# Kernel optimization log

Measured on AMD Instinct MI355X. Metric: run time of the kernel, lower is better.

The kernel has to match this reference:

```python
import jax, jax.numpy as jnp
import numpy as np
import math

D_IN, D_MODEL, N_HEADS, N_LAYERS, D_FF = 128, 256, 4, 4, 1024
NUM_BANDS = D_MODEL // 6  # 42 -> 252 encoding dims, zero-padded to 256
LN_EPS = 1e-5


def setup_inputs() -> dict:
    key = jax.random.key(0)
    ks = jax.random.split(key, 32)
    N, B = 65536, 128
    s = 0.02
    L, D, F = N_LAYERS, D_MODEL, D_FF
    inp = {
        "dom_embeddings": jax.random.normal(ks[0], (N, D_IN), jnp.float32),
        "dom_to_event_idx": jnp.sort(jax.random.randint(ks[1], (N,), 0, B)),
        "batch_size": B,
        "geometry": jax.random.normal(ks[2], (N, 3), jnp.float32),
        "in_proj_w": jax.random.normal(ks[3], (D, D_IN), jnp.float32) * s,
        "in_proj_b": jnp.zeros((D,), jnp.float32),
        "geo_proj_w": jax.random.normal(ks[4], (D, D), jnp.float32) * s,
        "geo_proj_b": jnp.zeros((D,), jnp.float32),
        "cls_token": jax.random.normal(ks[5], (1, 1, D), jnp.float32),
        "qkv_w": jax.random.normal(ks[6], (L, 3 * D, D), jnp.float32) * s,
        "qkv_b": jnp.zeros((L, 3 * D), jnp.float32),
        "out_w": jax.random.normal(ks[7], (L, D, D), jnp.float32) * s,
        "out_b": jnp.zeros((L, D), jnp.float32),
        "ln1_w": jnp.ones((L, D), jnp.float32),
        "ln1_b": jnp.zeros((L, D), jnp.float32),
        "ln2_w": jnp.ones((L, D), jnp.float32),
        "ln2_b": jnp.zeros((L, D), jnp.float32),
        "ff_w1": jax.random.normal(ks[8], (L, F, D), jnp.float32) * s,
        "ff_b1": jnp.zeros((L, F), jnp.float32),
        "ff_w2": jax.random.normal(ks[9], (L, D, F), jnp.float32) * s,
        "ff_b2": jnp.zeros((L, D), jnp.float32),
        "head_w1": jax.random.normal(ks[10], (D, D), jnp.float32) * s,
        "head_b1": jnp.zeros((D,), jnp.float32),
        "head_w2": jax.random.normal(ks[11], (2, D), jnp.float32) * s,
        "head_b2": jnp.zeros((2,), jnp.float32),
    }
    return inp


def _layer_norm(x, w, b):
    m = x.mean(-1, keepdims=True)
    v = ((x - m) ** 2).mean(-1, keepdims=True)
    return (x - m) / jnp.sqrt(v + LN_EPS) * w + b


def _pos_enc(geometry):
    # geometry: (N,3). Order: per coord -> per freq -> [sin, cos]; pad to D_MODEL.
    freqs = jnp.logspace(0.0, 1.0, NUM_BANDS, dtype=jnp.float32)  # 1..max_freq=10
    ang = 2.0 * math.pi * geometry[:, :, None] * freqs[None, None, :]  # (N,3,F)
    sc = jnp.stack([jnp.sin(ang), jnp.cos(ang)], axis=-1)  # (N,3,F,2)
    enc = sc.reshape(geometry.shape[0], 3 * NUM_BANDS * 2)  # (N,252)
    pad = D_MODEL - enc.shape[1]
    return jnp.pad(enc, ((0, 0), (0, pad)))


def _self_attn(x, pad_mask, Wqkv, bqkv, Wo, bo):
    B, S, D = x.shape
    H, hd = N_HEADS, D // N_HEADS
    qkv = x @ Wqkv.T + bqkv  # (B,S,3D)
    q, k, v = jnp.split(qkv, 3, axis=-1)
    q = q.reshape(B, S, H, hd).transpose(0, 2, 1, 3)
    k = k.reshape(B, S, H, hd).transpose(0, 2, 1, 3)
    v = v.reshape(B, S, H, hd).transpose(0, 2, 1, 3)
    scores = jnp.einsum('bhqd,bhkd->bhqk', q, k) / math.sqrt(hd)
    scores = jnp.where(pad_mask[:, None, None, :], -jnp.inf, scores)
    a = jax.nn.softmax(scores, axis=-1)
    o = jnp.einsum('bhqk,bhkd->bhqd', a, v).transpose(0, 2, 1, 3).reshape(B, S, D)
    return o @ Wo.T + bo


def reference(dom_embeddings, dom_to_event_idx, batch_size, geometry,
              in_proj_w, in_proj_b, geo_proj_w, geo_proj_b, cls_token,
              qkv_w, qkv_b, out_w, out_b, ln1_w, ln1_b, ln2_w, ln2_b,
              ff_w1, ff_b1, ff_w2, ff_b2, head_w1, head_b1, head_w2, head_b2):
    N = dom_embeddings.shape[0]
    B = int(batch_size)
    x = dom_embeddings @ in_proj_w.T + in_proj_b  # (N,D)
    geo = _pos_enc(geometry) @ geo_proj_w.T + geo_proj_b
    x = x + geo

    # Vectorized scatter-pack (replaces per-DOM Python loop).
    counts = jnp.bincount(dom_to_event_idx, length=B)
    starts = jnp.concatenate([jnp.zeros((1,), counts.dtype), jnp.cumsum(counts)[:-1]])
    pos = jnp.arange(N) - starts[dom_to_event_idx] + 1  # slot 0 reserved for CLS
    max_doms = int(counts.max())
    S = max_doms + 1

    batch_tensor = jnp.zeros((B, S, D_MODEL), x.dtype)
    batch_tensor = batch_tensor.at[:, 0, :].set(cls_token[0, 0])
    batch_tensor = batch_tensor.at[dom_to_event_idx, pos].set(x)
    # True = padded. NOTE: CLS slot stays True, faithful to original code.
    pad_mask = jnp.ones((B, S), bool).at[dom_to_event_idx, pos].set(False)

    h = batch_tensor
    for l in range(N_LAYERS):  # pre-LN encoder layers
        h = h + _self_attn(_layer_norm(h, ln1_w[l], ln1_b[l]), pad_mask,
                           qkv_w[l], qkv_b[l], out_w[l], out_b[l])
        ff_in = _layer_norm(h, ln2_w[l], ln2_b[l])
        h = h + jax.nn.relu(ff_in @ ff_w1[l].T + ff_b1[l]) @ ff_w2[l].T + ff_b2[l]

    cls = h[:, 0, :]
    hid = jax.nn.relu(cls @ head_w1.T + head_b1)
    return hid @ head_w2.T + head_b2  # (B,2)
```

## Files before the change

kernel.cpp:

```cpp
#include <hip/hip_runtime.h>
#include <hip/hip_bf16.h>
#include <math.h>


#define D_INPUT  128
#define DM       256
#define NHEADS   4
#define HDIM     64
#define NLAYERS  4
#define DFF      1024
#define BEV      128
#define LNEPS    1e-5f
#define KT       10
#define SCL      0.18033688011112042f

typedef unsigned short u16;
typedef __attribute__((ext_vector_type(8))) short bf16x8;
typedef __attribute__((ext_vector_type(4))) float f32x4;

__device__ inline u16 f2bf(float x) {
    unsigned int xi = __float_as_uint(x);
    unsigned int r  = xi + 0x7FFFu + ((xi >> 16) & 1u);
    return (u16)(r >> 16);
}
__device__ inline unsigned int cvtpk(float lo, float hi) {
    unsigned int r;
    asm("v_cvt_pk_bf16_f32 %0, %1, %2" : "=v"(r) : "v"(lo), "v"(hi));
    return r;
}

__device__ inline size_t apack(int row, int col, int nkt) {
    return ((size_t)(row >> 4) * nkt + (col >> 6)) * 1024
         + ((col >> 5) & 1) * 512
         + ((((col >> 3) & 3) * 16 + (row & 15)) * 8) + (col & 7);
}
__device__ inline size_t wpack_off(int col, int k, int nkt) {
    const int c16 = col >> 4, llo = col & 15;
    const int kt = k >> 6, kr = k & 63;
    const int kk = kr >> 5, lhi = (kr >> 3) & 3, e = kr & 7;
    return ((size_t)(c16 * nkt + kt)) * 1024 + kk * 512 + (lhi * 16 + llo) * 8 + e;
}


__global__ void starts_kernel(const int* __restrict__ idx, int* __restrict__ counts,
                              int* __restrict__ starts, int N) {
    __shared__ int bnd[BEV + 1];
    const int b = threadIdx.x;
    if (b <= BEV) {
        int lo = 0, hi = N;
        while (lo < hi) { int mid = (lo + hi) >> 1; if (idx[mid] < b) lo = mid + 1; else hi = mid; }
        bnd[b] = lo;
    }
    __syncthreads();
    if (b < BEV) { starts[b] = bnd[b]; counts[b] = bnd[b + 1] - bnd[b]; }
}

__global__ void r2bs_kernel(const int* __restrict__ idx, const int* __restrict__ starts,
                            int* __restrict__ r2bs, int N, int TP) {
    int i = blockIdx.x * blockDim.x + threadIdx.x;
    if (i < N) {
        int b = idx[i];
        r2bs[i] = (b << 16) | (i - starts[b] + 1);
    } else if (i < N + BEV) {
        r2bs[i] = (i - N) << 16;
    } else if (i < TP) {
        r2bs[i] = BEV << 16;
    }
}

__global__ void beacon_kernel(float* out, int n, float v) {
    int i = blockIdx.x * blockDim.x + threadIdx.x;
    if (i < n) out[i] = v;
}

__global__ void cvt4p_kernel(const float* __restrict__ s0, const float* __restrict__ s1,
                             const float* __restrict__ s2, const float* __restrict__ s3,
                             u16* __restrict__ d0, u16* __restrict__ d1,
                             u16* __restrict__ d2, u16* __restrict__ d3) {
    const int n0 = NLAYERS * 768 * 256, n1 = NLAYERS * 256 * 256;
    const int n2 = NLAYERS * 1024 * 256, n3 = NLAYERS * 256 * 1024;
    int i = blockIdx.x * blockDim.x + threadIdx.x;
    if (i < n0) {
        const int NoK = 768 * 256;
        int l = i / NoK, rem = i - l * NoK, col = rem >> 8, k = rem & 255;
        d0[(size_t)l * NoK + wpack_off(col, k, 4)] = f2bf(s0[i]);
        return;
    }
    i -= n0;
    if (i < n1) {
        const int NoK = 256 * 256;
        int l = i / NoK, rem = i - l * NoK, col = rem >> 8, k = rem & 255;
        d1[(size_t)l * NoK + wpack_off(col, k, 4)] = f2bf(s1[i]);
        return;
    }
    i -= n1;
    if (i < n2) {
        const int NoK = 1024 * 256;
        int l = i / NoK, rem = i - l * NoK, col = rem >> 8, k = rem & 255;
        d2[(size_t)l * NoK + wpack_off(col, k, 4)] = f2bf(s2[i]);
        return;
    }
    i -= n2;
    if (i < n3) {
        const int NoK = 256 * 1024;
        int l = i / NoK, rem = i - l * NoK, col = rem >> 10, k = rem & 1023;
        d3[(size_t)l * NoK + wpack_off(col, k, 16)] = f2bf(s3[i]);
    }
}

__global__ void prep_w_kernel(const float* __restrict__ win, const float* __restrict__ wgeo,
                              const float* __restrict__ bin, const float* __restrict__ bgeo,
                              u16* __restrict__ We, float* __restrict__ be) {
    int i = blockIdx.x * blockDim.x + threadIdx.x;
    if (i < 256 * 384) {
        int o = i / 384, k = i % 384;
        float v = 0.f;
        if (k < 128)      v = win[o * 128 + k];
        else if (k < 380) v = wgeo[o * 256 + (k - 128)];
        We[wpack_off(o, k, 6)] = f2bf(v);
    }
    if (i < 256) be[i] = bin[i] + bgeo[i];
}

__global__ void prep_a_kernel(const float* __restrict__ emb, const float* __restrict__ geo,
                              u16* __restrict__ Ap, int N) {
    size_t t = (size_t)blockIdx.x * blockDim.x + threadIdx.x;
    if (t >= (size_t)N * 96) return;
    const int c4 = (int)(t % 96) * 4;
    const size_t r = t / 96;
    float v[4];
    #pragma unroll
    for (int u = 0; u < 4; ++u) {
        const int k = c4 + u;
        float x = 0.f;
        if (k < 128) {
            x = emb[r * 128 + k];
        } else if (k < 380) {
            int rem  = k - 128;
            int axis = rem / 84;
            int r2   = rem % 84;
            int band = r2 >> 1;
            int sc   = r2 & 1;
            float freq = expf((float)band * (2.3025850929940457f / 41.0f));
            float ang  = (6.283185307179586f * geo[r * 3 + axis]) * freq;
            x = sc ? cosf(ang) : sinf(ang);
        }
        v[u] = x;
    }
    uint2 pp;
    pp.x = cvtpk(v[0], v[1]);
    pp.y = cvtpk(v[2], v[3]);
    *(uint2*)&Ap[apack((int)r, c4, 6)] = pp;
}

__global__ void cls_kernel(const float* __restrict__ cls, float* __restrict__ h, int N) {
    h[(size_t)(N + blockIdx.x) * DM + threadIdx.x] = cls[threadIdx.x];
}


__global__ __launch_bounds__(256) void ln_kernel(const float* __restrict__ x,
                                                 const float* __restrict__ w,
                                                 const float* __restrict__ b,
                                                 u16* __restrict__ yp, int T) {
    int row  = blockIdx.x * 4 + (threadIdx.x >> 6);
    int lane = threadIdx.x & 63;
    if (row >= T) return;
    float4 v = ((const float4*)(x + (size_t)row * DM))[lane];
    float s = v.x + v.y + v.z + v.w;
    #pragma unroll
    for (int off = 32; off > 0; off >>= 1) s += __shfl_xor(s, off);
    float mean = s * (1.0f / 256.0f);
    float dx = v.x - mean, dy = v.y - mean, dz = v.z - mean, dw = v.w - mean;
    float ss = dx * dx + dy * dy + dz * dz + dw * dw;
    #pragma unroll
    for (int off = 32; off > 0; off >>= 1) ss += __shfl_xor(ss, off);
    float inv = rsqrtf(ss * (1.0f / 256.0f) + LNEPS);
    float4 wv = ((const float4*)w)[lane];
    float4 bv = ((const float4*)b)[lane];
    const int col0 = lane * 4;
    uint2 yy;
    yy.x = cvtpk(dx * inv * wv.x + bv.x, dy * inv * wv.y + bv.y);
    yy.y = cvtpk(dz * inv * wv.z + bv.z, dw * inv * wv.w + bv.w);
    *(uint2*)&yp[apack(row, col0, 4)] = yy;
}


template <int MODE>
__global__ __launch_bounds__(256) void pgemm_kernel(const u16* __restrict__ Xp,
                                                    const u16* __restrict__ Wp,
                                                    const float* __restrict__ bias,
                                                    float* __restrict__ C,
                                                    u16* __restrict__ Qb,
                                                    u16* __restrict__ KVt,
                                                    const int* __restrict__ r2bs,
                                                    int nkt) {
    const int m0 = blockIdx.y * 64, n0 = blockIdx.x * 256;
    const int tid = threadIdx.x, wv = tid >> 6, lane = tid & 63;
    const int lhi = lane >> 4, llo = lane & 15;
    const int rt0 = m0 >> 4;

    f32x4 acc[4][4];
    #pragma unroll
    for (int i = 0; i < 4; ++i)
        #pragma unroll
        for (int j = 0; j < 4; ++j) acc[i][j] = (f32x4){0.f, 0.f, 0.f, 0.f};

    for (int kt = 0; kt < nkt; ++kt) {
        #pragma unroll
        for (int kk = 0; kk < 2; ++kk) {
            bf16x8 xf[4], wf[4];
            #pragma unroll
            for (int i = 0; i < 4; ++i)
                xf[i] = *(const bf16x8*)(Xp + ((size_t)(rt0 + i) * nkt + kt) * 1024
                                         + kk * 512 + lane * 8);
            #pragma unroll
            for (int j = 0; j < 4; ++j) {
                const int c16 = (n0 >> 4) + wv * 4 + j;
                wf[j] = *(const bf16x8*)(Wp + ((size_t)c16 * nkt + kt) * 1024
                                         + kk * 512 + lane * 8);
            }
            #pragma unroll
            for (int i = 0; i < 4; ++i)
                #pragma unroll
                for (int j = 0; j < 4; ++j)
                    acc[i][j] = __builtin_amdgcn_mfma_f32_16x16x32_bf16(wf[j], xf[i], acc[i][j], 0, 0, 0);
        }
    }

    #pragma unroll
    for (int i = 0; i < 4; ++i) {
        const int row = m0 + i * 16 + llo;
        int eb = 0, pos = 0, ktile = KT;
        if (MODE == 1 && n0 >= 256) {
            const int bs = r2bs[row];
            eb = bs >> 16; pos = bs & 0xffff; ktile = pos >> 6;
        }
        #pragma unroll
        for (int j = 0; j < 4; ++j) {
            const int col0 = n0 + wv * 64 + j * 16 + lhi * 4;
            const float4 bb = *(const float4*)&bias[col0];
            const float v0 = acc[i][j][0] + bb.x, v1 = acc[i][j][1] + bb.y;
            const float v2 = acc[i][j][2] + bb.z, v3 = acc[i][j][3] + bb.w;
            if (MODE == 0) {
                float4 c = {v0, v1, v2, v3};
                *(float4*)&C[(size_t)row * 256 + col0] = c;
            } else if (MODE == 2) {
                uint2 yy;
                yy.x = cvtpk(fmaxf(v0, 0.f), fmaxf(v1, 0.f));
                yy.y = cvtpk(fmaxf(v2, 0.f), fmaxf(v3, 0.f));
                *(uint2*)&Qb[apack(row, col0, 16)] = yy;
            } else if (n0 == 0) {
                uint2 q;
                q.x = cvtpk(v0 * SCL, v1 * SCL);
                q.y = cvtpk(v2 * SCL, v3 * SCL);
                *(uint2*)&Qb[(size_t)row * 256 + col0] = q;
            } else if (n0 == 256) {
                if (ktile < KT) {
                    const int dg = col0 - 256, hh = dg >> 6, d0 = dg & 63;
                    const int unit = ((pos & 63) >> 4) * 2 + (d0 >> 5);
                    const int lt = ((d0 >> 3) & 3) * 16 + (pos & 15);
                    uint2 pp = {cvtpk(v0, v1), cvtpk(v2, v3)};
                    *(uint2*)&KVt[(((size_t)(eb * 4 + hh) * 2 + 0) * KT + ktile) * 4096
                                  + unit * 512 + lt * 8 + (d0 & 7)] = pp;
                }
            } else {
                if (ktile < KT) {
                    const int dg = col0 - 512, hh = dg >> 6, d0 = dg & 63;
                    const size_t vb = (((size_t)(eb * 4 + hh) * 2 + 1) * KT + ktile) * 4096
                                    + ((d0 >> 4) * 2 + ((pos & 63) >> 5)) * 512
                                    + ((((pos & 63) >> 3) & 3) * 16) * 8 + (pos & 7);
                    KVt[vb + (size_t)((d0 & 15) + 0) * 8] = f2bf(v0);
                    KVt[vb + (size_t)((d0 & 15) + 1) * 8] = f2bf(v1);
                    KVt[vb + (size_t)((d0 & 15) + 2) * 8] = f2bf(v2);
                    KVt[vb + (size_t)((d0 & 15) + 3) * 8] = f2bf(v3);
                }
            }
        }
    }
}


__global__ __launch_bounds__(256) void mgemmln_kernel(const u16* __restrict__ Xp,
                                                      const u16* __restrict__ Wp,
                                                      const float* __restrict__ bias,
                                                      float* __restrict__ H,
                                                      const float* __restrict__ lnw,
                                                      const float* __restrict__ lnb,
                                                      u16* __restrict__ Yp,
                                                      int nkt) {
    __shared__ float part[2][4][64];
    const int m0 = blockIdx.x * 64;
    const int tid = threadIdx.x, wv = tid >> 6, lane = tid & 63;
    const int lhi = lane >> 4, llo = lane & 15;
    const int rt0 = m0 >> 4;

    f32x4 acc[4][4];
    #pragma unroll
    for (int i = 0; i < 4; ++i)
        #pragma unroll
        for (int j = 0; j < 4; ++j) acc[i][j] = (f32x4){0.f, 0.f, 0.f, 0.f};

    for (int kt = 0; kt < nkt; ++kt) {
        #pragma unroll
        for (int kk = 0; kk < 2; ++kk) {
            bf16x8 xf[4], wf[4];
            #pragma unroll
            for (int i = 0; i < 4; ++i)
                xf[i] = *(const bf16x8*)(Xp + ((size_t)(rt0 + i) * nkt + kt) * 1024
                                         + kk * 512 + lane * 8);
            #pragma unroll
            for (int j = 0; j < 4; ++j) {
                const int c16 = wv * 4 + j;
                wf[j] = *(const bf16x8*)(Wp + ((size_t)c16 * nkt + kt) * 1024
                                         + kk * 512 + lane * 8);
            }
            #pragma unroll
            for (int i = 0; i < 4; ++i)
                #pragma unroll
                for (int j = 0; j < 4; ++j)
                    acc[i][j] = __builtin_amdgcn_mfma_f32_16x16x32_bf16(wf[j], xf[i], acc[i][j], 0, 0, 0);
        }
    }

    float rsum[4], rsq[4];
    #pragma unroll
    for (int i = 0; i < 4; ++i) { rsum[i] = 0.f; rsq[i] = 0.f; }
    #pragma unroll
    for (int i = 0; i < 4; ++i) {
        const int row = m0 + i * 16 + llo;
        #pragma unroll
        for (int j = 0; j < 4; ++j) {
            const int col0 = wv * 64 + j * 16 + lhi * 4;
            const float4 bb = *(const float4*)&bias[col0];
            const float4 hv = *(const float4*)&H[(size_t)row * DM + col0];
            float v0 = acc[i][j][0] + bb.x + hv.x;
            float v1 = acc[i][j][1] + bb.y + hv.y;
            float v2 = acc[i][j][2] + bb.z + hv.z;
            float v3 = acc[i][j][3] + bb.w + hv.w;
            acc[i][j][0] = v0; acc[i][j][1] = v1; acc[i][j][2] = v2; acc[i][j][3] = v3;
            rsum[i] += (v0 + v1) + (v2 + v3);
            rsq[i]  += (v0 * v0 + v1 * v1) + (v2 * v2 + v3 * v3);
        }
    }
    #pragma unroll
    for (int i = 0; i < 4; ++i) {
        rsum[i] += __shfl_xor(rsum[i], 16);  rsum[i] += __shfl_xor(rsum[i], 32);
        rsq[i]  += __shfl_xor(rsq[i], 16);   rsq[i]  += __shfl_xor(rsq[i], 32);
    }
    __syncthreads();
    if (lhi == 0) {
        #pragma unroll
        for (int i = 0; i < 4; ++i) {
            const int rl = i * 16 + llo;
            part[0][wv][rl] = rsum[i];
            part[1][wv][rl] = rsq[i];
        }
    }
    __syncthreads();

    #pragma unroll
    for (int i = 0; i < 4; ++i) {
        const int rl = i * 16 + llo;
        const int row = m0 + rl;
        const float s = (part[0][0][rl] + part[0][1][rl]) + (part[0][2][rl] + part[0][3][rl]);
        const float q = (part[1][0][rl] + part[1][1][rl]) + (part[1][2][rl] + part[1][3][rl]);
        const float mean = s * (1.0f / 256.0f);
        const float var  = fmaxf(q * (1.0f / 256.0f) - mean * mean, 0.f);
        const float rstd = rsqrtf(var + LNEPS);
        #pragma unroll
        for (int j = 0; j < 4; ++j) {
            const int col0 = wv * 64 + j * 16 + lhi * 4;
            const float4 wl = *(const float4*)&lnw[col0];
            const float4 bl = *(const float4*)&lnb[col0];
            float4 hv;
            hv.x = acc[i][j][0]; hv.y = acc[i][j][1];
            hv.z = acc[i][j][2]; hv.w = acc[i][j][3];
            *(float4*)&H[(size_t)row * DM + col0] = hv;
            uint2 yy;
            yy.x = cvtpk((hv.x - mean) * rstd * wl.x + bl.x,
                         (hv.y - mean) * rstd * wl.y + bl.y);
            yy.y = cvtpk((hv.z - mean) * rstd * wl.z + bl.z,
                         (hv.w - mean) * rstd * wl.w + bl.w);
            *(uint2*)&Yp[apack(row, col0, 4)] = yy;
        }
    }
}


__global__ __launch_bounds__(256) void mattn_kernel(const u16* __restrict__ Qb,
                                                    const u16* __restrict__ KVt,
                                                    const int* __restrict__ counts,
                                                    const int* __restrict__ starts,
                                                    u16* __restrict__ outp, int N) {
    const int id  = blockIdx.x;
    const int rem = id >> 3;
    const int qt  = rem % KT;
    const int bh  = (rem / KT) * 8 + (id & 7);
    const int b = bh >> 2, hh = bh & 3;
    const int Sb = counts[b] + 1;
    const int qbase = qt * 64;
    if (qbase >= Sb) return;
    const int start = starts[b];
    __shared__ u16 Pl[4][16 * 72];
    const int tid = threadIdx.x;
    const int w = tid >> 6, lane = tid & 63;
    const int llo = lane & 15, lhi = lane >> 4;

    const int qi = qbase + w * 16 + llo;
    const size_t qrow = (qi < Sb && qi > 0) ? (size_t)(start + qi - 1) : (size_t)(N + b);
    bf16x8 bq[2];
    bq[0] = *(const bf16x8*)(Qb + qrow * 256 + hh * 64 + lhi * 8);
    bq[1] = *(const bf16x8*)(Qb + qrow * 256 + hh * 64 + 32 + lhi * 8);

    const u16* kb = KVt + ((size_t)bh * 2 + 0) * KT * 4096;
    const u16* vb = KVt + ((size_t)bh * 2 + 1) * KT * 4096;

    f32x4 acc[4];
    #pragma unroll
    for (int i = 0; i < 4; ++i) acc[i] = (f32x4){0.f, 0.f, 0.f, 0.f};
    float m = -1e30f, l = 0.f;

    int nt = (Sb + 63) >> 6;
    if (nt > KT) nt = KT;

    for (int t = 0; t < nt; ++t) {
        const int kbase = t * 64;
        const u16* kp = kb + t * 4096 + lane * 8;
        const u16* vp = vb + t * 4096 + lane * 8;

        bf16x8 ak[4][2], av[4][2];
        #pragma unroll
        for (int i = 0; i < 4; ++i) {
            #pragma unroll
            for (int kk = 0; kk < 2; ++kk) {
                ak[i][kk] = *(const bf16x8*)(kp + (i * 2 + kk) * 512);
                av[i][kk] = *(const bf16x8*)(vp + (i * 2 + kk) * 512);
            }
        }

        f32x4 sc[4];
        #pragma unroll
        for (int i = 0; i < 4; ++i) sc[i] = (f32x4){0.f, 0.f, 0.f, 0.f};
        __builtin_amdgcn_s_setprio(1);
        #pragma unroll
        for (int kk = 0; kk < 2; ++kk)
            #pragma unroll
            for (int i = 0; i < 4; ++i)
                sc[i] = __builtin_amdgcn_mfma_f32_16x16x32_bf16(ak[i][kk], bq[kk], sc[i], 0, 0, 0);
        __builtin_amdgcn_s_setprio(0);

        float rm;
        if (kbase + 64 <= Sb) {
            float m0v = fmaxf(fmaxf(sc[0][0], sc[0][1]), fmaxf(sc[0][2], sc[0][3]));
            float m1v = fmaxf(fmaxf(sc[1][0], sc[1][1]), fmaxf(sc[1][2], sc[1][3]));
            float m2v = fmaxf(fmaxf(sc[2][0], sc[2][1]), fmaxf(sc[2][2], sc[2][3]));
            float m3v = fmaxf(fmaxf(sc[3][0], sc[3][1]), fmaxf(sc[3][2], sc[3][3]));
            rm = fmaxf(fmaxf(m0v, m1v), fmaxf(m2v, m3v));
        } else {
            rm = -1e30f;
            #pragma unroll
            for (int i = 0; i < 4; ++i)
                #pragma unroll
                for (int r = 0; r < 4; ++r) {
                    const int key = kbase + i * 16 + lhi * 4 + r;
                    const float s = (key < Sb) ? sc[i][r] : -1e30f;
                    sc[i][r] = s;
                    rm = fmaxf(rm, s);
                }
        }
        rm = fmaxf(rm, __shfl_xor(rm, 16));
        rm = fmaxf(rm, __shfl_xor(rm, 32));

        if (!__all(rm <= m + 8.f)) {
            const float mnew = fmaxf(m, rm);
            const float corr = exp2f(m - mnew);
            l *= corr;
            #pragma unroll
            for (int i = 0; i < 4; ++i) acc[i] *= corr;
            m = mnew;
        }

        float ls = 0.f;
        #pragma unroll
        for (int i = 0; i < 4; ++i) {
            const float p0 = exp2f(sc[i][0] - m), p1 = exp2f(sc[i][1] - m);
            const float p2 = exp2f(sc[i][2] - m), p3 = exp2f(sc[i][3] - m);
            ls += (p0 + p1) + (p2 + p3);
            uint2 pp;
            pp.x = cvtpk(p0, p1);
            pp.y = cvtpk(p2, p3);
            *(uint2*)&Pl[w][llo * 72 + i * 16 + lhi * 4] = pp;
        }
        ls += __shfl_xor(ls, 16);
        ls += __shfl_xor(ls, 32);
        l += ls;

        __builtin_amdgcn_s_setprio(1);
        #pragma unroll
        for (int kk = 0; kk < 2; ++kk) {
            bf16x8 pb = *(const bf16x8*)&Pl[w][llo * 72 + kk * 32 + lhi * 8];
            #pragma unroll
            for (int i = 0; i < 4; ++i)
                acc[i] = __builtin_amdgcn_mfma_f32_16x16x32_bf16(av[i][kk], pb, acc[i], 0, 0, 0);
        }
        __builtin_amdgcn_s_setprio(0);
    }

    if (qi < Sb) {
        const size_t orow = (qi == 0) ? (size_t)(N + b) : (size_t)(start + qi - 1);
        const float invl = 1.f / l;
        #pragma unroll
        for (int i = 0; i < 4; ++i) {
            const int col0 = hh * 64 + i * 16 + lhi * 4;
            uint2 yy;
            yy.x = cvtpk(acc[i][0] * invl, acc[i][1] * invl);
            yy.y = cvtpk(acc[i][2] * invl, acc[i][3] * invl);
            *(uint2*)&outp[apack((int)orow, col0, 4)] = yy;
        }
    }
}


__global__ __launch_bounds__(256) void head_kernel(const float* __restrict__ h,
                                                   const float* __restrict__ w1,
                                                   const float* __restrict__ b1,
                                                   const float* __restrict__ w2,
                                                   const float* __restrict__ b2,
                                                   float* __restrict__ out, int N) {
    const int b = blockIdx.x;
    const int t = threadIdx.x;
    __shared__ float cls[DM];
    __shared__ float hid[DM];
    cls[t] = h[(size_t)(N + b) * DM + t];
    __syncthreads();
    float s = b1[t];
    for (int k = 0; k < DM; ++k) s = fmaf(cls[k], w1[t * DM + k], s);
    hid[t] = fmaxf(s, 0.f);
    __syncthreads();
    if (t < 2) {
        float o = b2[t];
        for (int k = 0; k < DM; ++k) o = fmaf(hid[k], w2[t * DM + k], o);
        out[b * 2 + t] = o;
    }
}


extern "C" void kernel_launch(void* const* d_in, const int* in_sizes, int n_in,
                              void* d_out, int out_size, void* d_ws, size_t ws_size,
                              hipStream_t stream) {
    const float* dom_emb   = (const float*)d_in[0];
    const int*   dom_idx   = (const int*)d_in[1];
    const float* geometry  = (const float*)d_in[3];
    const float* in_w      = (const float*)d_in[4];
    const float* in_b      = (const float*)d_in[5];
    const float* geo_w     = (const float*)d_in[6];
    const float* geo_b     = (const float*)d_in[7];
    const float* cls_tok   = (const float*)d_in[8];
    const float* qkv_w     = (const float*)d_in[9];
    const float* qkv_b     = (const float*)d_in[10];
    const float* out_w     = (const float*)d_in[11];
    const float* out_b     = (const float*)d_in[12];
    const float* ln1_w     = (const float*)d_in[13];
    const float* ln1_b     = (const float*)d_in[14];
    const float* ln2_w     = (const float*)d_in[15];
    const float* ln2_b     = (const float*)d_in[16];
    const float* ff_w1     = (const float*)d_in[17];
    const float* ff_b1     = (const float*)d_in[18];
    const float* ff_w2     = (const float*)d_in[19];
    const float* ff_b2     = (const float*)d_in[20];
    const float* head_w1   = (const float*)d_in[21];
    const float* head_b1   = (const float*)d_in[22];
    const float* head_w2   = (const float*)d_in[23];
    const float* head_b2   = (const float*)d_in[24];
    float* outp = (float*)d_out;

    const int N  = in_sizes[0] / D_INPUT;
    const int T  = N + BEV;
    const int TP = ((T + 255) / 256) * 256;

    char* base = (char*)d_ws;
    size_t off = 0;
    int* counts = (int*)(base + off);          off += 1024;
    int* starts = (int*)(base + off);          off += 1024;
    u16*   Web  = (u16*)(base + off);          off += (size_t)256 * 384 * 2;
    float* be   = (float*)(base + off);        off += 1024;
    u16*   wq   = (u16*)(base + off);          off += (size_t)NLAYERS * 768 * 256 * 2;
    u16*   wo   = (u16*)(base + off);          off += (size_t)NLAYERS * 256 * 256 * 2;
    u16*   w1b  = (u16*)(base + off);          off += (size_t)NLAYERS * 1024 * 256 * 2;
    u16*   w2b  = (u16*)(base + off);          off += (size_t)NLAYERS * 256 * 1024 * 2;
    int*   r2bs = (int*)(base + off);          off += ((size_t)TP * 4 + 255) & ~255ULL;
    float* h    = (float*)(base + off);        off += (size_t)TP * DM * 4;
    u16*   xb   = (u16*)(base + off);          off += (size_t)TP * DM * 2;
    const size_t qb_sz  = (size_t)TP * 256 * 2;
    const size_t kvt_sz = (size_t)(BEV + 1) * 4 * 2 * KT * 4096 * 2;
    char* bigc = base + off;                   off += qb_sz + kvt_sz;
    u16* Ab   = (u16*)bigc;
    u16* Qbuf = (u16*)bigc;
    u16* KVt  = (u16*)(bigc + qb_sz);
    u16* ffm  = (u16*)bigc;

    if (ws_size < off) {
        beacon_kernel<<<1, 256, 0, stream>>>(outp, out_size, (float)(ws_size >> 20));
        return;
    }

    {
        const int ntot = NLAYERS * (768 * 256 + 256 * 256 + 1024 * 256 + 256 * 1024);
        cvt4p_kernel<<<(ntot + 255) / 256, 256, 0, stream>>>(
            qkv_w, out_w, ff_w1, ff_w2, wq, wo, w1b, w2b);
    }
    prep_w_kernel<<<(256 * 384 + 255) / 256, 256, 0, stream>>>(in_w, geo_w, in_b, geo_b, Web, be);

    starts_kernel<<<1, 256, 0, stream>>>(dom_idx, counts, starts, N);
    r2bs_kernel<<<(TP + 255) / 256, 256, 0, stream>>>(dom_idx, starts, r2bs, N, TP);

    prep_a_kernel<<<(int)(((size_t)N * 96 + 255) / 256), 256, 0, stream>>>(dom_emb, geometry, Ab, N);
    pgemm_kernel<0><<<dim3(1, N / 64), 256, 0, stream>>>(
        Ab, Web, be, h, nullptr, nullptr, nullptr, 6);
    cls_kernel<<<BEV, DM, 0, stream>>>(cls_tok, h, N);

    ln_kernel<<<TP / 4, 256, 0, stream>>>(h, ln1_w, ln1_b, xb, TP);
    for (int l = 0; l < NLAYERS; ++l) {
        pgemm_kernel<1><<<dim3(3, TP / 64), 256, 0, stream>>>(
            xb, wq + (size_t)l * 768 * 256, qkv_b + l * 768, nullptr, Qbuf, KVt, r2bs, 4);
        mattn_kernel<<<8 * KT * (BEV * NHEADS / 8), 256, 0, stream>>>(
            Qbuf, KVt, counts, starts, xb, N);
        mgemmln_kernel<<<TP / 64, 256, 0, stream>>>(
            xb, wo + (size_t)l * 256 * 256, out_b + l * DM, h,
            ln2_w + l * DM, ln2_b + l * DM, xb, 4);
        const int lnx = (l + 1 < NLAYERS) ? (l + 1) : l;
        for (int c = 0; c < 2; ++c) {
            const int r0 = c * (TP / 2);
            const u16* xc = xb + ((size_t)(r0 >> 4)) * 4 * 1024;
            pgemm_kernel<2><<<dim3(4, TP / 128), 256, 0, stream>>>(
                xc, w1b + (size_t)l * DFF * 256, ff_b1 + l * DFF, nullptr, ffm,
                nullptr, nullptr, 4);
            mgemmln_kernel<<<TP / 128, 256, 0, stream>>>(
                ffm, w2b + (size_t)l * 256 * DFF, ff_b2 + l * DM, h + (size_t)r0 * DM,
                ln1_w + lnx * DM, ln1_b + lnx * DM,
                xb + ((size_t)(r0 >> 4)) * 4 * 1024, 16);
        }
    }

    head_kernel<<<BEV, DM, 0, stream>>>(h, head_w1, head_b1, head_w2, head_b2, outp, N);
}
```

Baseline: 1.714 ms.

## Process two query fragments per attention block and use nontemporal residual loads/stores

The attention kernel now handles 128 queries per block (two 64-query fragments per wave set) instead of 64, so each K/V tile loaded into registers is reused for two query fragments and half as many blocks reload K/V. The grid shrinks accordingly. Separately, the out-projection+LN kernel reads and writes the residual stream with nontemporal loads/stores to reduce cache pollution. The attention change raises register pressure (double accumulators) and reduces block count, which may lower occupancy or waste work on partial trailing query tiles.

Measured after the change: 1.825 ms. +6.5%, slower.

```diff
diff --git a/kernel.cpp b/kernel.cpp
--- a/kernel.cpp
+++ b/kernel.cpp
@@ -12,6 +12,7 @@
 #define BEV      128
 #define LNEPS    1e-5f
 #define KT       10
+#define QTQ      5
 #define SCL      0.18033688011112042f
 
 typedef unsigned short u16;
@@ -332,11 +333,11 @@
         for (int j = 0; j < 4; ++j) {
             const int col0 = wv * 64 + j * 16 + lhi * 4;
             const float4 bb = *(const float4*)&bias[col0];
-            const float4 hv = *(const float4*)&H[(size_t)row * DM + col0];
-            float v0 = acc[i][j][0] + bb.x + hv.x;
-            float v1 = acc[i][j][1] + bb.y + hv.y;
-            float v2 = acc[i][j][2] + bb.z + hv.z;
-            float v3 = acc[i][j][3] + bb.w + hv.w;
+            const f32x4 hv = __builtin_nontemporal_load((const f32x4*)&H[(size_t)row * DM + col0]);
+            float v0 = acc[i][j][0] + bb.x + hv[0];
+            float v1 = acc[i][j][1] + bb.y + hv[1];
+            float v2 = acc[i][j][2] + bb.z + hv[2];
+            float v3 = acc[i][j][3] + bb.w + hv[3];
             acc[i][j][0] = v0; acc[i][j][1] = v1; acc[i][j][2] = v2; acc[i][j][3] = v3;
             rsum[i] += (v0 + v1) + (v2 + v3);
             rsq[i]  += (v0 * v0 + v1 * v1) + (v2 * v2 + v3 * v3);
@@ -372,15 +373,15 @@
             const int col0 = wv * 64 + j * 16 + lhi * 4;
             const float4 wl = *(const float4*)&lnw[col0];
             const float4 bl = *(const float4*)&lnb[col0];
-            float4 hv;
-            hv.x = acc[i][j][0]; hv.y = acc[i][j][1];
-            hv.z = acc[i][j][2]; hv.w = acc[i][j][3];
-            *(float4*)&H[(size_t)row * DM + col0] = hv;
+            f32x4 hv;
+            hv[0] = acc[i][j][0]; hv[1] = acc[i][j][1];
+            hv[2] = acc[i][j][2]; hv[3] = acc[i][j][3];
+            __builtin_nontemporal_store(hv, (f32x4*)&H[(size_t)row * DM + col0]);
             uint2 yy;
-            yy.x = cvtpk((hv.x - mean) * rstd * wl.x + bl.x,
-                         (hv.y - mean) * rstd * wl.y + bl.y);
-            yy.y = cvtpk((hv.z - mean) * rstd * wl.z + bl.z,
-                         (hv.w - mean) * rstd * wl.w + bl.w);
+            yy.x = cvtpk((hv[0] - mean) * rstd * wl.x + bl.x,
+                         (hv[1] - mean) * rstd * wl.y + bl.y);
+            yy.y = cvtpk((hv[2] - mean) * rstd * wl.z + bl.z,
+                         (hv[3] - mean) * rstd * wl.w + bl.w);
             *(uint2*)&Yp[apack(row, col0, 4)] = yy;
         }
     }
@@ -394,11 +395,11 @@
                                                     u16* __restrict__ outp, int N) {
     const int id  = blockIdx.x;
     const int rem = id >> 3;
-    const int qt  = rem % KT;
-    const int bh  = (rem / KT) * 8 + (id & 7);
+    const int qt  = rem % QTQ;
+    const int bh  = (rem / QTQ) * 8 + (id & 7);
     const int b = bh >> 2, hh = bh & 3;
     const int Sb = counts[b] + 1;
-    const int qbase = qt * 64;
+    const int qbase = qt * 128;
     if (qbase >= Sb) return;
     const int start = starts[b];
     __shared__ u16 Pl[4][16 * 72];
@@ -406,19 +407,26 @@
     const int w = tid >> 6, lane = tid & 63;
     const int llo = lane & 15, lhi = lane >> 4;
 
-    const int qi = qbase + w * 16 + llo;
-    const size_t qrow = (qi < Sb && qi > 0) ? (size_t)(start + qi - 1) : (size_t)(N + b);
-    bf16x8 bq[2];
-    bq[0] = *(const bf16x8*)(Qb + qrow * 256 + hh * 64 + lhi * 8);
-    bq[1] = *(const bf16x8*)(Qb + qrow * 256 + hh * 64 + 32 + lhi * 8);
+    int qi[2];
+    size_t qrow[2];
+    bf16x8 bq[2][2];
+    #pragma unroll
+    for (int qf = 0; qf < 2; ++qf) {
+        qi[qf] = qbase + qf * 64 + w * 16 + llo;
+        qrow[qf] = (qi[qf] < Sb && qi[qf] > 0) ? (size_t)(start + qi[qf] - 1) : (size_t)(N + b);
+        bq[qf][0] = *(const bf16x8*)(Qb + qrow[qf] * 256 + hh * 64 + lhi * 8);
+        bq[qf][1] = *(const bf16x8*)(Qb + qrow[qf] * 256 + hh * 64 + 32 + lhi * 8);
+    }
 
     const u16* kb = KVt + ((size_t)bh * 2 + 0) * KT * 4096;
     const u16* vb = KVt + ((size_t)bh * 2 + 1) * KT * 4096;
 
-    f32x4 acc[4];
-    #pragma unroll
-    for (int i = 0; i < 4; ++i) acc[i] = (f32x4){0.f, 0.f, 0.f, 0.f};
-    float m = -1e30f, l = 0.f;
+    f32x4 acc[2][4];
+    #pragma unroll
+    for (int qf = 0; qf < 2; ++qf)
+        #pragma unroll
+        for (int i = 0; i < 4; ++i) acc[qf][i] = (f32x4){0.f, 0.f, 0.f, 0.f};
+    float m[2] = {-1e30f, -1e30f}, l[2] = {0.f, 0.f};
 
     int nt = (Sb + 63) >> 6;
     if (nt > KT) nt = KT;
@@ -437,85 +445,92 @@
                 av[i][kk] = *(const bf16x8*)(vp + (i * 2 + kk) * 512);
             }
         }
-
-        f32x4 sc[4];
-        #pragma unroll
-        for (int i = 0; i < 4; ++i) sc[i] = (f32x4){0.f, 0.f, 0.f, 0.f};
-        __builtin_amdgcn_s_setprio(1);
-        #pragma unroll
-        for (int kk = 0; kk < 2; ++kk)
-            #pragma unroll
-            for (int i = 0; i < 4; ++i)
-                sc[i] = __builtin_amdgcn_mfma_f32_16x16x32_bf16(ak[i][kk], bq[kk], sc[i], 0, 0, 0);
-        __builtin_amdgcn_s_setprio(0);
-
-        float rm;
-        if (kbase + 64 <= Sb) {
-            float m0v = fmaxf(fmaxf(sc[0][0], sc[0][1]), fmaxf(sc[0][2], sc[0][3]));
-            float m1v = fmaxf(fmaxf(sc[1][0], sc[1][1]), fmaxf(sc[1][2], sc[1][3]));
-            float m2v = fmaxf(fmaxf(sc[2][0], sc[2][1]), fmaxf(sc[2][2], sc[2][3]));
-            float m3v = fmaxf(fmaxf(sc[3][0], sc[3][1]), fmaxf(sc[3][2], sc[3][3]));
-            rm = fmaxf(fmaxf(m0v, m1v), fmaxf(m2v, m3v));
-        } else {
-            rm = -1e30f;
-            #pragma unroll
-            for (int i = 0; i < 4; ++i)
+        const bool fullTile = (kbase + 64 <= Sb);
+
+        #pragma unroll
+        for (int qf = 0; qf < 2; ++qf) {
+            f32x4 sc[4];
+            #pragma unroll
+            for (int i = 0; i < 4; ++i) sc[i] = (f32x4){0.f, 0.f, 0.f, 0.f};
+            __builtin_amdgcn_s_setprio(1);
+            #pragma unroll
+            for (int kk = 0; kk < 2; ++kk)
                 #pragma unroll
-                for (int r = 0; r < 4; ++r) {
-                    const int key = kbase + i * 16 + lhi * 4 + r;
-                    const float s = (key < Sb) ? sc[i][r] : -1e30f;
-                    sc[i][r] = s;
-                    rm = fmaxf(rm, s);
-                }
-        }
-        rm = fmaxf(rm, __shfl_xor(rm, 16));
-        rm = fmaxf(rm, __shfl_xor(rm, 32));
-
-        if (!__all(rm <= m + 8.f)) {
-            const float mnew = fmaxf(m, rm);
-            const float corr = exp2f(m - mnew);
-            l *= corr;
-            #pragma unroll
-            for (int i = 0; i < 4; ++i) acc[i] *= corr;
-            m = mnew;
-        }
-
-        float ls = 0.f;
-        #pragma unroll
-        for (int i = 0; i < 4; ++i) {
-            const float p0 = exp2f(sc[i][0] - m), p1 = exp2f(sc[i][1] - m);
-            const float p2 = exp2f(sc[i][2] - m), p3 = exp2f(sc[i][3] - m);
-            ls += (p0 + p1) + (p2 + p3);
-            uint2 pp;
-            pp.x = cvtpk(p0, p1);
-            pp.y = cvtpk(p2, p3);
-            *(uint2*)&Pl[w][llo * 72 + i * 16 + lhi * 4] = pp;
-        }
-        ls += __shfl_xor(ls, 16);
-        ls += __shfl_xor(ls, 32);
-        l += ls;
-
-        __builtin_amdgcn_s_setprio(1);
-        #pragma unroll
-        for (int kk = 0; kk < 2; ++kk) {
-            bf16x8 pb = *(const bf16x8*)&Pl[w][llo * 72 + kk * 32 + lhi * 8];
-            #pragma unroll
-            for (int i = 0; i < 4; ++i)
-                acc[i] = __builtin_amdgcn_mfma_f32_16x16x32_bf16(av[i][kk], pb, acc[i], 0, 0, 0);
-        }
-        __builtin_amdgcn_s_setprio(0);
-    }
-
-    if (qi < Sb) {
-        const size_t orow = (qi == 0) ? (size_t)(N + b) : (size_t)(start + qi - 1);
-        const float invl = 1.f / l;
-        #pragma unroll
-        for (int i = 0; i < 4; ++i) {
-            const int col0 = hh * 64 + i * 16 + lhi * 4;
-            uint2 yy;
-            yy.x = cvtpk(acc[i][0] * invl, acc[i][1] * invl);
-            yy.y = cvtpk(acc[i][2] * invl, acc[i][3] * invl);
-            *(uint2*)&outp[apack((int)orow, col0, 4)] = yy;
+                for (int i = 0; i < 4; ++i)
+                    sc[i] = __builtin_amdgcn_mfma_f32_16x16x32_bf16(ak[i][kk], bq[qf][kk], sc[i], 0, 0, 0);
+            __builtin_amdgcn_s_setprio(0);
+
+            float rm;
+            if (fullTile) {
+                float m0v = fmaxf(fmaxf(sc[0][0], sc[0][1]), fmaxf(sc[0][2], sc[0][3]));
+                float m1v = fmaxf(fmaxf(sc[1][0], sc[1][1]), fmaxf(sc[1][2], sc[1][3]));
+                float m2v = fmaxf(fmaxf(sc[2][0], sc[2][1]), fmaxf(sc[2][2], sc[2][3]));
+                float m3v = fmaxf(fmaxf(sc[3][0], sc[3][1]), fmaxf(sc[3][2], sc[3][3]));
+                rm = fmaxf(fmaxf(m0v, m1v), fmaxf(m2v, m3v));
+            } else {
+                rm = -1e30f;
+                #pragma unroll
+                for (int i = 0; i < 4; ++i)
+                    #pragma unroll
+                    for (int r = 0; r < 4; ++r) {
+                        const int key = kbase + i * 16 + lhi * 4 + r;
+                        const float s = (key < Sb) ? sc[i][r] : -1e30f;
+                        sc[i][r] = s;
+                        rm = fmaxf(rm, s);
+                    }
+            }
+            rm = fmaxf(rm, __shfl_xor(rm, 16));
+            rm = fmaxf(rm, __shfl_xor(rm, 32));
+
+            if (!__all(rm <= m[qf] + 8.f)) {
+                const float mnew = fmaxf(m[qf], rm);
+                const float corr = exp2f(m[qf] - mnew);
+                l[qf] *= corr;
+                #pragma unroll
+                for (int i = 0; i < 4; ++i) acc[qf][i] *= corr;
+                m[qf] = mnew;
+            }
+
+            float ls = 0.f;
+            #pragma unroll
+            for (int i = 0; i < 4; ++i) {
+                const float p0 = exp2f(sc[i][0] - m[qf]), p1 = exp2f(sc[i][1] - m[qf]);
+                const float p2 = exp2f(sc[i][2] - m[qf]), p3 = exp2f(sc[i][3] - m[qf]);
+                ls += (p0 + p1) + (p2 + p3);
+                uint2 pp;
+                pp.x = cvtpk(p0, p1);
+                pp.y = cvtpk(p2, p3);
+                *(uint2*)&Pl[w][llo * 72 + i * 16 + lhi * 4] = pp;
+            }
+            ls += __shfl_xor(ls, 16);
+            ls += __shfl_xor(ls, 32);
+            l[qf] += ls;
+
+            __builtin_amdgcn_s_setprio(1);
+            #pragma unroll
+            for (int kk = 0; kk < 2; ++kk) {
+                bf16x8 pb = *(const bf16x8*)&Pl[w][llo * 72 + kk * 32 + lhi * 8];
+                #pragma unroll
+                for (int i = 0; i < 4; ++i)
+                    acc[qf][i] = __builtin_amdgcn_mfma_f32_16x16x32_bf16(av[i][kk], pb, acc[qf][i], 0, 0, 0);
+            }
+            __builtin_amdgcn_s_setprio(0);
+        }
+    }
+
+    #pragma unroll
+    for (int qf = 0; qf < 2; ++qf) {
+        if (qi[qf] < Sb) {
+            const size_t orow = (qi[qf] == 0) ? (size_t)(N + b) : (size_t)(start + qi[qf] - 1);
+            const float invl = 1.f / l[qf];
+            #pragma unroll
+            for (int i = 0; i < 4; ++i) {
+                const int col0 = hh * 64 + i * 16 + lhi * 4;
+                uint2 yy;
+                yy.x = cvtpk(acc[qf][i][0] * invl, acc[qf][i][1] * invl);
+                yy.y = cvtpk(acc[qf][i][2] * invl, acc[qf][i][3] * invl);
+                *(uint2*)&outp[apack((int)orow, col0, 4)] = yy;
+            }
         }
     }
 }
@@ -623,7 +638,7 @@
     for (int l = 0; l < NLAYERS; ++l) {
         pgemm_kernel<1><<<dim3(3, TP / 64), 256, 0, stream>>>(
             xb, wq + (size_t)l * 768 * 256, qkv_b + l * 768, nullptr, Qbuf, KVt, r2bs, 4);
-        mattn_kernel<<<8 * KT * (BEV * NHEADS / 8), 256, 0, stream>>>(
+        mattn_kernel<<<8 * QTQ * (BEV * NHEADS / 8), 256, 0, stream>>>(
             Qbuf, KVt, counts, starts, xb, N);
         mgemmln_kernel<<<TP / 64, 256, 0, stream>>>(
             xb, wo + (size_t)l * 256 * 256, out_b + l * DM, h,
```
